# Optimization experiments

Measured on AMD Instinct MI355X. Metric: run time of the kernel, lower is better.

Reference implementation:

```python
import jax, jax.numpy as jnp
import numpy as np

THRESHOLD = 20.0
CIRCLE_OFFSETS = [(0, -3), (1, -3), (2, -2), (3, -1), (3, 0), (3, 1), (2, 2), (1, 3),
                  (0, 3), (-1, 3), (-2, 2), (-3, 1), (-3, 0), (-3, -1), (-2, -2), (-1, -3)]


def setup_inputs() -> dict:
    key = jax.random.key(0)
    image = jax.random.uniform(key, (4, 1, 1080, 1920), dtype=jnp.float32) * 255.0
    return {"image": image}


def _detect_9_consecutive(bits_16):
    # bits_16: int32 (N, H, W). Build 24-bit circular buffer, test all 16 rotations
    # for 9 consecutive set bits (window == 511) using arithmetic-only ops.
    lower_8 = bits_16 % 256
    buffer_24 = bits_16 + lower_8 * 65536  # (N, H, W) int32
    divisors = (jnp.int32(2) ** jnp.arange(16, dtype=jnp.int32)).reshape(16, 1, 1, 1)
    shifted = (buffer_24[None] // divisors) % 512  # (16, N, H, W)
    return jnp.any(shifted == 511, axis=0)  # (N, H, W) bool


def reference(image):
    N, C, H, W = image.shape
    img = image.astype(jnp.float32)
    # Replicate-pad by 3 and gather the 16 Bresenham circle pixels via shifted slices.
    padded = jnp.pad(img[:, 0], ((0, 0), (3, 3), (3, 3)), mode='edge')  # (N, H+6, W+6)
    circle = jnp.stack(
        [padded[:, 3 + dy:3 + dy + H, 3 + dx:3 + dx + W] for dy, dx in CIRCLE_OFFSETS],
        axis=-1)  # (N, H, W, 16)
    center = img[:, 0][..., None]  # (N, H, W, 1)
    diff = circle - center
    powers = (jnp.int32(1) << jnp.arange(16, dtype=jnp.int32)).reshape(1, 1, 1, 16)
    dark_bits = ((diff >= THRESHOLD).astype(jnp.int32) * powers).sum(axis=-1)
    bright_bits = ((diff <= -THRESHOLD).astype(jnp.int32) * powers).sum(axis=-1)
    detected = _detect_9_consecutive(dark_bits) | _detect_9_consecutive(bright_bits)
    return detected.astype(jnp.float32)[:, None]  # (N, 1, H, W)
```

## Files before the change

kernel.cpp:

```cpp
#include <hip/hip_runtime.h>

#define IMG_H 1080
#define IMG_W 1920
#define TILE_W 64
#define TILE_H 4
#define SW 70
#define SH 10
#define SP 72

__device__ __forceinline__ unsigned det9(unsigned m) {
    unsigned x = m | (m << 16);
    unsigned t = x & (x >> 1);
    t &= t >> 2;
    t &= t >> 4;
    t &= x >> 8;
    return t;
}

__global__ __launch_bounds__(256) void fast_score_kernel(const float* __restrict__ img,
                                                         float* __restrict__ out) {
    __shared__ float sm[SH * SP];

    const int n  = blockIdx.z;
    const int x0 = blockIdx.x * TILE_W;
    const int y0 = blockIdx.y * TILE_H;
    const int tid = threadIdx.x;

    const float* in = img + (size_t)n * (IMG_H * IMG_W);
    float* op = out + (size_t)n * (IMG_H * IMG_W);

    for (int i = tid; i < SH * SW; i += 256) {
        const int r = i / SW;
        const int c = i - r * SW;
        int gy = min(max(y0 - 3 + r, 0), IMG_H - 1);
        int gx = min(max(x0 - 3 + c, 0), IMG_W - 1);
        sm[r * SP + c] = in[(size_t)gy * IMG_W + gx];
    }
    __syncthreads();

    const int tx = tid & 63;
    const int ty = tid >> 6;
    const float* base = &sm[(ty + 3) * SP + (tx + 3)];

    constexpr int DY[16] = {0, 1, 2, 3, 3, 3, 2, 1, 0, -1, -2, -3, -3, -3, -2, -1};
    constexpr int DX[16] = {-3, -3, -2, -1, 0, 1, 2, 3, 3, 3, 2, 1, 0, -1, -2, -3};

    const float center = base[0];
    float t[16];
#pragma unroll
    for (int k = 0; k < 16; ++k) {
        t[k] = base[DY[k] * SP + DX[k]];
    }

    const float hi = center + 20.0f;
    const float lo = center - 20.0f;
    unsigned dark = 0u, bright = 0u;
#pragma unroll
    for (int k = 0; k < 16; ++k) {
        dark   |= (t[k] >= hi ? 1u : 0u) << k;
        bright |= (t[k] <= lo ? 1u : 0u) << k;
    }

    const float res = (det9(dark) | det9(bright)) ? 1.0f : 0.0f;
    op[(size_t)(y0 + ty) * IMG_W + (x0 + tx)] = res;
}

extern "C" void kernel_launch(void* const* d_in, const int* in_sizes, int n_in,
                              void* d_out, int out_size, void* d_ws, size_t ws_size,
                              hipStream_t stream) {
    const float* img = (const float*)d_in[0];
    float* out = (float*)d_out;
    const int n_img = in_sizes[0] / (IMG_H * IMG_W);
    dim3 grid(IMG_W / TILE_W,
              IMG_H / TILE_H,
              n_img);
    fast_score_kernel<<<grid, 256, 0, stream>>>(img, out);
}
```

Measured before the change: 110.9 us.

## Replace shared-memory tiles with per-thread vertical register sliding window

Drops the shared-memory staging and barrier. Each thread now owns one column and walks 16 rows, keeping the 7-column circle neighbourhood in rotating register arrays so each row step needs only 7 new global loads. Horizontal neighbour reuse is left to the L1/L2 caches, and boundary clamping is done with per-column and per-row min/max. The cost is more global load instructions, higher register pressure and half-idle blocks in the last x-column, since 1920 is not a multiple of 256.

```diff
diff --git a/kernel.cpp b/kernel.cpp
--- a/kernel.cpp
+++ b/kernel.cpp
@@ -2,11 +2,7 @@
 
 #define IMG_H 1080
 #define IMG_W 1920
-#define TILE_W 64
-#define TILE_H 4
-#define SW 70
-#define SH 10
-#define SP 72
+#define SY 16
 
 __device__ __forceinline__ unsigned det9(unsigned m) {
     unsigned x = m | (m << 16);
@@ -19,50 +15,66 @@
 
 __global__ __launch_bounds__(256) void fast_score_kernel(const float* __restrict__ img,
                                                          float* __restrict__ out) {
-    __shared__ float sm[SH * SP];
+    const int n  = blockIdx.z;
+    const int gx = blockIdx.x * 256 + threadIdx.x;
+    const int y0 = blockIdx.y * SY;
 
-    const int n  = blockIdx.z;
-    const int x0 = blockIdx.x * TILE_W;
-    const int y0 = blockIdx.y * TILE_H;
-    const int tid = threadIdx.x;
+    const float* base = img + (size_t)n * (IMG_H * IMG_W);
+    float* ob = out + (size_t)n * (IMG_H * IMG_W);
 
-    const float* in = img + (size_t)n * (IMG_H * IMG_W);
-    float* op = out + (size_t)n * (IMG_H * IMG_W);
+    int c[7];
+#pragma unroll
+    for (int d = 0; d < 7; ++d) c[d] = min(max(gx + d - 3, 0), IMG_W - 1);
 
-    for (int i = tid; i < SH * SW; i += 256) {
-        const int r = i / SW;
-        const int c = i - r * SW;
-        int gy = min(max(y0 - 3 + r, 0), IMG_H - 1);
-        int gx = min(max(x0 - 3 + c, 0), IMG_W - 1);
-        sm[r * SP + c] = in[(size_t)gy * IMG_W + gx];
-    }
-    __syncthreads();
+#define ROWP(r) (base + (size_t)min(max((r), 0), IMG_H - 1) * IMG_W)
 
-    const int tx = tid & 63;
-    const int ty = tid >> 6;
-    const float* base = &sm[(ty + 3) * SP + (tx + 3)];
-
-    constexpr int DY[16] = {0, 1, 2, 3, 3, 3, 2, 1, 0, -1, -2, -3, -3, -3, -2, -1};
-    constexpr int DX[16] = {-3, -3, -2, -1, 0, 1, 2, 3, 3, 3, 2, 1, 0, -1, -2, -3};
-
-    const float center = base[0];
-    float t[16];
+    float L[3], Rr[3], a2m[5], a2p[5], a1m[7], a1p[7], a0[7];
 #pragma unroll
-    for (int k = 0; k < 16; ++k) {
-        t[k] = base[DY[k] * SP + DX[k]];
+    for (int i = 0; i < 3; ++i) { L[i]   = ROWP(y0 - 1 + i)[c[0]]; Rr[i]  = ROWP(y0 - 1 + i)[c[6]]; }
+#pragma unroll
+    for (int i = 0; i < 5; ++i) { a2m[i] = ROWP(y0 - 2 + i)[c[1]]; a2p[i] = ROWP(y0 - 2 + i)[c[5]]; }
+#pragma unroll
+    for (int i = 0; i < 7; ++i) {
+        a1m[i] = ROWP(y0 - 3 + i)[c[2]];
+        a0[i]  = ROWP(y0 - 3 + i)[c[3]];
+        a1p[i] = ROWP(y0 - 3 + i)[c[4]];
     }
 
-    const float hi = center + 20.0f;
-    const float lo = center - 20.0f;
-    unsigned dark = 0u, bright = 0u;
 #pragma unroll
-    for (int k = 0; k < 16; ++k) {
-        dark   |= (t[k] >= hi ? 1u : 0u) << k;
-        bright |= (t[k] <= lo ? 1u : 0u) << k;
+    for (int j = 0; j < SY; ++j) {
+        const int y = y0 + j;
+
+        const float nl  = ROWP(y + 2)[c[0]];
+        const float nr  = ROWP(y + 2)[c[6]];
+        const float n2m = ROWP(y + 3)[c[1]];
+        const float n2p = ROWP(y + 3)[c[5]];
+        const float n1m = ROWP(y + 4)[c[2]];
+        const float n0c = ROWP(y + 4)[c[3]];
+        const float n1p = ROWP(y + 4)[c[4]];
+
+        const float center = a0[3];
+        const float hi = center + 20.0f;
+        const float lo = center - 20.0f;
+        const float t[16] = {L[1], L[2], a2m[4], a1m[6], a0[6], a1p[6], a2p[4], Rr[2],
+                             Rr[1], Rr[0], a2p[0], a1p[0], a0[0], a1m[0], a2m[0], L[0]};
+        unsigned dark = 0u, bright = 0u;
+#pragma unroll
+        for (int k = 0; k < 16; ++k) {
+            dark   = (dark << 1)   + (t[k] >= hi ? 1u : 0u);
+            bright = (bright << 1) + (t[k] <= lo ? 1u : 0u);
+        }
+        const float res = (det9(dark) | det9(bright)) ? 1.0f : 0.0f;
+        if (gx < IMG_W && y < IMG_H) ob[(size_t)y * IMG_W + gx] = res;
+
+        L[0] = L[1];  L[1] = L[2];  L[2] = nl;
+        Rr[0] = Rr[1]; Rr[1] = Rr[2]; Rr[2] = nr;
+        a2m[0] = a2m[1]; a2m[1] = a2m[2]; a2m[2] = a2m[3]; a2m[3] = a2m[4]; a2m[4] = n2m;
+        a2p[0] = a2p[1]; a2p[1] = a2p[2]; a2p[2] = a2p[3]; a2p[3] = a2p[4]; a2p[4] = n2p;
+        a1m[0] = a1m[1]; a1m[1] = a1m[2]; a1m[2] = a1m[3]; a1m[3] = a1m[4]; a1m[4] = a1m[5]; a1m[5] = a1m[6]; a1m[6] = n1m;
+        a1p[0] = a1p[1]; a1p[1] = a1p[2]; a1p[2] = a1p[3]; a1p[3] = a1p[4]; a1p[4] = a1p[5]; a1p[5] = a1p[6]; a1p[6] = n1p;
+        a0[0]  = a0[1];  a0[1]  = a0[2];  a0[2]  = a0[3];  a0[3]  = a0[4];  a0[4]  = a0[5];  a0[5]  = a0[6];  a0[6]  = n0c;
     }
-
-    const float res = (det9(dark) | det9(bright)) ? 1.0f : 0.0f;
-    op[(size_t)(y0 + ty) * IMG_W + (x0 + tx)] = res;
+#undef ROWP
 }
 
 extern "C" void kernel_launch(void* const* d_in, const int* in_sizes, int n_in,
@@ -71,8 +83,8 @@
     const float* img = (const float*)d_in[0];
     float* out = (float*)d_out;
     const int n_img = in_sizes[0] / (IMG_H * IMG_W);
-    dim3 grid(IMG_W / TILE_W,
-              IMG_H / TILE_H,
+    dim3 grid((IMG_W + 255) / 256,
+              (IMG_H + SY - 1) / SY,
               n_img);
     fast_score_kernel<<<grid, 256, 0, stream>>>(img, out);
 }
```

After: 103.8 us. 1.07x faster.
